# Optimization experiments

Hardware: AMD Instinct MI355X
Metric: run time of the kernel (lower is better)

The kernel has to match this reference:

```python
import jax, jax.numpy as jnp
import numpy as np

HUGE_FLOAT = 1000.0
B, LATENT, N, EMB, NBOND = 256, 256, 64, 64, 5


def setup_inputs() -> dict:
    key = jax.random.key(0)
    ks = jax.random.split(key, 8)
    s1 = 1.0 / np.sqrt(LATENT)
    s2 = 1.0 / np.sqrt(2 * EMB)
    s3 = 1.0 / np.sqrt(EMB)
    return {
        "z": jax.random.normal(ks[0], (B, LATENT), dtype=jnp.float32),
        "num_real_atoms": jax.random.randint(ks[1], (B,), 1, N + 1, dtype=jnp.int32),
        "W_nodes": jax.random.uniform(ks[2], (LATENT, N * EMB), jnp.float32, -s1, s1),
        "b_nodes": jax.random.uniform(ks[3], (N * EMB,), jnp.float32, -s1, s1),
        "W1": jax.random.uniform(ks[4], (2 * EMB, EMB), jnp.float32, -s2, s2),
        "b1": jax.random.uniform(ks[5], (EMB,), jnp.float32, -s2, s2),
        "W2": jax.random.uniform(ks[6], (EMB, NBOND), jnp.float32, -s3, s3),
        "b2": jax.random.uniform(ks[7], (NBOND,), jnp.float32, -s3, s3),
    }


def reference(z, num_real_atoms, W_nodes, b_nodes, W1, b1, W2, b2):
    # z: (B, latent) -> node embeddings h: (B, N, emb)
    h = (z @ W_nodes + b_nodes).reshape(B, N, EMB)
    # edge MLP first layer on concat([h_i, h_j]) == h_i @ W1a + h_j @ W1b
    W1a, W1b = W1[:EMB], W1[EMB:]
    a = jnp.einsum("bne,ef->bnf", h, W1a)  # (B, N, emb)
    c = jnp.einsum("bne,ef->bnf", h, W1b)  # (B, N, emb)
    hidden = jax.nn.relu(a[:, :, None, :] + c[:, None, :, :] + b1)  # (B,N,N,emb)
    logits = jnp.einsum("bijf,fk->bijk", hidden, W2) + b2  # (B,N,N,5)
    # diagonal mask + padding mask (symmetric), constant fill per bond channel
    diag = jnp.eye(N, dtype=bool)  # (N,N)
    real = jnp.arange(N)[None, :] < num_real_atoms[:, None]  # (B,N)
    pad = ~real
    padding = pad[:, :, None] | pad[:, None, :]  # (B,N,N)
    mask = diag[None] | padding  # (B,N,N)
    fill = jnp.where(jnp.arange(NBOND) == NBOND - 1, HUGE_FLOAT, -HUGE_FLOAT).astype(logits.dtype)
    logits = jnp.where(mask[..., None], fill, logits)
    # symmetrize over node pair dims
    return 0.5 * (logits + jnp.swapaxes(logits, 1, 2))
```

## Files before the change

### kernel.cpp

```cpp
#include <hip/hip_runtime.h>
#include <hip/hip_bf16.h>

#define HUGEF 1000.0f

typedef __hip_bfloat16 bf16;

__device__ __forceinline__ float b2f(bf16 x) { return __bfloat162float(x); }

__global__ __launch_bounds__(256) void k_hac(
    const float* __restrict__ z, const float* __restrict__ Wn,
    const float* __restrict__ bn, const float* __restrict__ W1,
    const float* __restrict__ b1, bf16* __restrict__ a_ws,
    bf16* __restrict__ c_ws)
{
    __shared__ float buf0[64][68];
    __shared__ float buf1[64][68];
    __shared__ float buf2[64][68];

    const int t = threadIdx.x;
    const int tx = t & 15, ty = t >> 4;
    const int atom = blockIdx.x;
    const int m0 = blockIdx.y * 64;
    const int n0 = atom * 64;

    float acc[4][4] = {};
    for (int k0 = 0; k0 < 256; k0 += 64) {
        __syncthreads();
        #pragma unroll
        for (int r = 0; r < 4; ++r) {
            int q = t + 256 * r;
            int m = q >> 4, kk = (q & 15) * 4;
            *(float4*)&buf0[m][kk] = *(const float4*)&z[(m0 + m) * 256 + k0 + kk];
        }
        #pragma unroll
        for (int r = 0; r < 4; ++r) {
            int q = t + 256 * r;
            int k = q >> 4, nn = (q & 15) * 4;
            *(float4*)&buf1[k][nn] = *(const float4*)&Wn[(k0 + k) * 4096 + n0 + nn];
        }
        __syncthreads();
        for (int k = 0; k < 64; ++k) {
            float4 bv = *(const float4*)&buf1[k][tx * 4];
            float bb[4] = {bv.x, bv.y, bv.z, bv.w};
            float aa[4];
            #pragma unroll
            for (int i = 0; i < 4; ++i) aa[i] = buf0[ty * 4 + i][k];
            #pragma unroll
            for (int i = 0; i < 4; ++i)
                #pragma unroll
                for (int jj = 0; jj < 4; ++jj) acc[i][jj] += aa[i] * bb[jj];
        }
    }
    __syncthreads();

    {
        float bnv[4];
        #pragma unroll
        for (int jj = 0; jj < 4; ++jj) bnv[jj] = bn[n0 + tx * 4 + jj];
        #pragma unroll
        for (int i = 0; i < 4; ++i)
            #pragma unroll
            for (int jj = 0; jj < 4; ++jj)
                buf2[ty * 4 + i][tx * 4 + jj] = acc[i][jj] + bnv[jj];
        #pragma unroll
        for (int r = 0; r < 4; ++r) {
            int q = t + 256 * r;
            int e = q >> 4, ff = (q & 15) * 4;
            *(float4*)&buf0[e][ff] = *(const float4*)&W1[4 * q];
            *(float4*)&buf1[e][ff] = *(const float4*)&W1[4096 + 4 * q];
        }
    }
    __syncthreads();

    float aacc[4][4] = {}, cacc[4][4] = {};
    const int b0 = ty * 4, f0 = tx * 4;
    for (int e = 0; e < 64; ++e) {
        float4 wa = *(const float4*)&buf0[e][f0];
        float4 wb = *(const float4*)&buf1[e][f0];
        float wav[4] = {wa.x, wa.y, wa.z, wa.w};
        float wbv[4] = {wb.x, wb.y, wb.z, wb.w};
        #pragma unroll
        for (int i = 0; i < 4; ++i) {
            float hv = buf2[b0 + i][e];
            #pragma unroll
            for (int jj = 0; jj < 4; ++jj) {
                aacc[i][jj] += hv * wav[jj];
                cacc[i][jj] += hv * wbv[jj];
            }
        }
    }
    float b1v[4];
    #pragma unroll
    for (int jj = 0; jj < 4; ++jj) b1v[jj] = b1[f0 + jj];
    #pragma unroll
    for (int i = 0; i < 4; ++i) {
        int bi = m0 + b0 + i;
        int idx = bi * 4096 + n0 + f0;
        ushort4 av, cv;
        av.x = __bfloat16_as_ushort(__float2bfloat16(aacc[i][0] + b1v[0]));
        av.y = __bfloat16_as_ushort(__float2bfloat16(aacc[i][1] + b1v[1]));
        av.z = __bfloat16_as_ushort(__float2bfloat16(aacc[i][2] + b1v[2]));
        av.w = __bfloat16_as_ushort(__float2bfloat16(aacc[i][3] + b1v[3]));
        cv.x = __bfloat16_as_ushort(__float2bfloat16(cacc[i][0]));
        cv.y = __bfloat16_as_ushort(__float2bfloat16(cacc[i][1]));
        cv.z = __bfloat16_as_ushort(__float2bfloat16(cacc[i][2]));
        cv.w = __bfloat16_as_ushort(__float2bfloat16(cacc[i][3]));
        *(ushort4*)&a_ws[idx] = av;
        *(ushort4*)&c_ws[idx] = cv;
    }
}

__global__ __launch_bounds__(256) void k_pairs(
    const bf16* __restrict__ a_ws, const bf16* __restrict__ c_ws,
    const int* __restrict__ nra, const float* __restrict__ W2,
    const float* __restrict__ b2, float* __restrict__ out)
{
    __shared__ float as[64][68];
    __shared__ float cs[64][68];
    __shared__ float w2t[5][68];

    const int t = threadIdx.x;
    const int bid = blockIdx.x;
    const int b = bid >> 2;
    const int ic = bid & 3;
    const int n = nra[b];

    #pragma unroll
    for (int r = 0; r < 4; ++r) {
        int q = t + 256 * r;
        int atom = q >> 4, ff = (q & 15) * 4;
        ushort4 av = *(const ushort4*)&a_ws[b * 4096 + 4 * q];
        ushort4 cv = *(const ushort4*)&c_ws[b * 4096 + 4 * q];
        as[atom][ff + 0] = b2f(__ushort_as_bfloat16(av.x));
        as[atom][ff + 1] = b2f(__ushort_as_bfloat16(av.y));
        as[atom][ff + 2] = b2f(__ushort_as_bfloat16(av.z));
        as[atom][ff + 3] = b2f(__ushort_as_bfloat16(av.w));
        cs[atom][ff + 0] = b2f(__ushort_as_bfloat16(cv.x));
        cs[atom][ff + 1] = b2f(__ushort_as_bfloat16(cv.y));
        cs[atom][ff + 2] = b2f(__ushort_as_bfloat16(cv.z));
        cs[atom][ff + 3] = b2f(__ushort_as_bfloat16(cv.w));
    }
    if (t < 64) {
        #pragma unroll
        for (int k = 0; k < 5; ++k) w2t[k][t] = W2[t * 5 + k];
    }
    float b2v[5];
    #pragma unroll
    for (int k = 0; k < 5; ++k) b2v[k] = b2[k];
    __syncthreads();

    const int j = t & 63;
    const int wq = t >> 6;
    const float fillv[5] = {-HUGEF, -HUGEF, -HUGEF, -HUGEF, HUGEF};

    #pragma unroll 1
    for (int q = 0; q < 4; ++q) {
        const int i = ic * 16 + wq * 4 + q;
        float* op = out + ((b * 64 + i) * 64 + j) * 5;
        if (i >= n) {
            #pragma unroll
            for (int k = 0; k < 5; ++k) op[k] = fillv[k];
            continue;
        }
        float acc[5] = {0.f, 0.f, 0.f, 0.f, 0.f};
        for (int f4 = 0; f4 < 64; f4 += 4) {
            float4 ai = *(const float4*)&as[i][f4];
            float4 ci = *(const float4*)&cs[i][f4];
            float4 aj = *(const float4*)&as[j][f4];
            float4 cj = *(const float4*)&cs[j][f4];
            float s0 = fmaxf(ai.x + cj.x, 0.f) + fmaxf(aj.x + ci.x, 0.f);
            float s1 = fmaxf(ai.y + cj.y, 0.f) + fmaxf(aj.y + ci.y, 0.f);
            float s2 = fmaxf(ai.z + cj.z, 0.f) + fmaxf(aj.z + ci.z, 0.f);
            float s3 = fmaxf(ai.w + cj.w, 0.f) + fmaxf(aj.w + ci.w, 0.f);
            #pragma unroll
            for (int k = 0; k < 5; ++k) {
                float4 w = *(const float4*)&w2t[k][f4];
                acc[k] += s0 * w.x + s1 * w.y + s2 * w.z + s3 * w.w;
            }
        }
        const bool masked = (j == i) || (j >= n);
        #pragma unroll
        for (int k = 0; k < 5; ++k) {
            float v = masked ? fillv[k] : (0.5f * acc[k] + b2v[k]);
            op[k] = v;
        }
    }
}

extern "C" void kernel_launch(void* const* d_in, const int* in_sizes, int n_in,
                              void* d_out, int out_size, void* d_ws, size_t ws_size,
                              hipStream_t stream)
{
    const float* z  = (const float*)d_in[0];
    const int*   nra = (const int*)d_in[1];
    const float* Wn = (const float*)d_in[2];
    const float* bn = (const float*)d_in[3];
    const float* W1 = (const float*)d_in[4];
    const float* b1 = (const float*)d_in[5];
    const float* W2 = (const float*)d_in[6];
    const float* b2 = (const float*)d_in[7];
    float* out = (float*)d_out;

    bf16* a_ws = (bf16*)d_ws;
    bf16* c_ws = a_ws + 256 * 4096;

    hipLaunchKernelGGL(k_hac, dim3(64, 4), dim3(256), 0, stream,
                       z, Wn, bn, W1, b1, a_ws, c_ws);
    hipLaunchKernelGGL(k_pairs, dim3(1024), dim3(256), 0, stream,
                       a_ws, c_ws, nra, W2, b2, out);
}
```

Measured before the change: 118.4 us.

## Prefetch GEMM tiles into registers, transpose smem for float4 reads, block pair loop

In the node/edge GEMM kernel, the next z and W_nodes tiles are prefetched into registers while the current tile is computed. z and h are stored transposed in shared memory so the inner loops can use float4 loads instead of strided scalar loads, and the inner loops are unrolled. In the pair kernel, each thread now handles four i-rows together, so the j-row and W2 loads are shared across them. Fully padded row groups exit early, and launch bounds request 4 blocks per CU. The cost is more registers per thread and bank conflicts from the transposed scalar shared-memory stores.

```diff
diff --git a/kernel.cpp b/kernel.cpp
--- a/kernel.cpp
+++ b/kernel.cpp
@@ -13,9 +13,9 @@
     const float* __restrict__ b1, bf16* __restrict__ a_ws,
     bf16* __restrict__ c_ws)
 {
-    __shared__ float buf0[64][68];
-    __shared__ float buf1[64][68];
-    __shared__ float buf2[64][68];
+    __shared__ __align__(16) float buf0[64][68];
+    __shared__ __align__(16) float buf1[64][68];
+    __shared__ __align__(16) float buf2[64][68];
 
     const int t = threadIdx.x;
     const int tx = t & 15, ty = t >> 4;
@@ -23,6 +23,16 @@
     const int m0 = blockIdx.y * 64;
     const int n0 = atom * 64;
 
+    float4 zr[4], wr[4];
+    #pragma unroll
+    for (int r = 0; r < 4; ++r) {
+        int q = t + 256 * r;
+        int m = q >> 4, kk = (q & 15) * 4;
+        zr[r] = *(const float4*)&z[(m0 + m) * 256 + 0 + kk];
+        int k = q >> 4, nn = (q & 15) * 4;
+        wr[r] = *(const float4*)&Wn[(0 + k) * 4096 + n0 + nn];
+    }
+
     float acc[4][4] = {};
     for (int k0 = 0; k0 < 256; k0 += 64) {
         __syncthreads();
@@ -30,21 +40,30 @@
         for (int r = 0; r < 4; ++r) {
             int q = t + 256 * r;
             int m = q >> 4, kk = (q & 15) * 4;
-            *(float4*)&buf0[m][kk] = *(const float4*)&z[(m0 + m) * 256 + k0 + kk];
-        }
-        #pragma unroll
-        for (int r = 0; r < 4; ++r) {
-            int q = t + 256 * r;
+            buf0[kk + 0][m] = zr[r].x;
+            buf0[kk + 1][m] = zr[r].y;
+            buf0[kk + 2][m] = zr[r].z;
+            buf0[kk + 3][m] = zr[r].w;
             int k = q >> 4, nn = (q & 15) * 4;
-            *(float4*)&buf1[k][nn] = *(const float4*)&Wn[(k0 + k) * 4096 + n0 + nn];
+            *(float4*)&buf1[k][nn] = wr[r];
+        }
+        if (k0 + 64 < 256) {
+            #pragma unroll
+            for (int r = 0; r < 4; ++r) {
+                int q = t + 256 * r;
+                int m = q >> 4, kk = (q & 15) * 4;
+                zr[r] = *(const float4*)&z[(m0 + m) * 256 + (k0 + 64) + kk];
+                int k = q >> 4, nn = (q & 15) * 4;
+                wr[r] = *(const float4*)&Wn[(k0 + 64 + k) * 4096 + n0 + nn];
+            }
         }
         __syncthreads();
+        #pragma unroll 4
         for (int k = 0; k < 64; ++k) {
+            float4 av = *(const float4*)&buf0[k][ty * 4];
             float4 bv = *(const float4*)&buf1[k][tx * 4];
+            float aa[4] = {av.x, av.y, av.z, av.w};
             float bb[4] = {bv.x, bv.y, bv.z, bv.w};
-            float aa[4];
-            #pragma unroll
-            for (int i = 0; i < 4; ++i) aa[i] = buf0[ty * 4 + i][k];
             #pragma unroll
             for (int i = 0; i < 4; ++i)
                 #pragma unroll
@@ -61,7 +80,7 @@
         for (int i = 0; i < 4; ++i)
             #pragma unroll
             for (int jj = 0; jj < 4; ++jj)
-                buf2[ty * 4 + i][tx * 4 + jj] = acc[i][jj] + bnv[jj];
+                buf2[tx * 4 + jj][ty * 4 + i] = acc[i][jj] + bnv[jj];
         #pragma unroll
         for (int r = 0; r < 4; ++r) {
             int q = t + 256 * r;
@@ -74,18 +93,20 @@
 
     float aacc[4][4] = {}, cacc[4][4] = {};
     const int b0 = ty * 4, f0 = tx * 4;
+    #pragma unroll 4
     for (int e = 0; e < 64; ++e) {
         float4 wa = *(const float4*)&buf0[e][f0];
         float4 wb = *(const float4*)&buf1[e][f0];
+        float4 hv4 = *(const float4*)&buf2[e][b0];
         float wav[4] = {wa.x, wa.y, wa.z, wa.w};
         float wbv[4] = {wb.x, wb.y, wb.z, wb.w};
+        float hv[4] = {hv4.x, hv4.y, hv4.z, hv4.w};
         #pragma unroll
         for (int i = 0; i < 4; ++i) {
-            float hv = buf2[b0 + i][e];
             #pragma unroll
             for (int jj = 0; jj < 4; ++jj) {
-                aacc[i][jj] += hv * wav[jj];
-                cacc[i][jj] += hv * wbv[jj];
+                aacc[i][jj] += hv[i] * wav[jj];
+                cacc[i][jj] += hv[i] * wbv[jj];
             }
         }
     }
@@ -110,14 +131,14 @@
     }
 }
 
-__global__ __launch_bounds__(256) void k_pairs(
+__global__ __launch_bounds__(256, 4) void k_pairs(
     const bf16* __restrict__ a_ws, const bf16* __restrict__ c_ws,
     const int* __restrict__ nra, const float* __restrict__ W2,
     const float* __restrict__ b2, float* __restrict__ out)
 {
-    __shared__ float as[64][68];
-    __shared__ float cs[64][68];
-    __shared__ float w2t[5][68];
+    __shared__ __align__(16) float as[64][68];
+    __shared__ __align__(16) float cs[64][68];
+    __shared__ __align__(16) float w2t[5][68];
 
     const int t = threadIdx.x;
     const int bid = blockIdx.x;
@@ -151,38 +172,56 @@
 
     const int j = t & 63;
     const int wq = t >> 6;
+    const int i0 = ic * 16 + wq * 4;
     const float fillv[5] = {-HUGEF, -HUGEF, -HUGEF, -HUGEF, HUGEF};
 
-    #pragma unroll 1
-    for (int q = 0; q < 4; ++q) {
-        const int i = ic * 16 + wq * 4 + q;
-        float* op = out + ((b * 64 + i) * 64 + j) * 5;
-        if (i >= n) {
+    if (i0 >= n) {
+        #pragma unroll
+        for (int r = 0; r < 4; ++r) {
+            float* op = out + ((b * 64 + i0 + r) * 64 + j) * 5;
             #pragma unroll
             for (int k = 0; k < 5; ++k) op[k] = fillv[k];
-            continue;
-        }
-        float acc[5] = {0.f, 0.f, 0.f, 0.f, 0.f};
-        for (int f4 = 0; f4 < 64; f4 += 4) {
-            float4 ai = *(const float4*)&as[i][f4];
-            float4 ci = *(const float4*)&cs[i][f4];
-            float4 aj = *(const float4*)&as[j][f4];
-            float4 cj = *(const float4*)&cs[j][f4];
+        }
+        return;
+    }
+
+    float acc[4][5] = {};
+    for (int f4 = 0; f4 < 64; f4 += 4) {
+        float4 aj = *(const float4*)&as[j][f4];
+        float4 cj = *(const float4*)&cs[j][f4];
+        float4 w0 = *(const float4*)&w2t[0][f4];
+        float4 w1 = *(const float4*)&w2t[1][f4];
+        float4 w2 = *(const float4*)&w2t[2][f4];
+        float4 w3 = *(const float4*)&w2t[3][f4];
+        float4 w4 = *(const float4*)&w2t[4][f4];
+        #pragma unroll
+        for (int r = 0; r < 4; ++r) {
+            float4 ai = *(const float4*)&as[i0 + r][f4];
+            float4 ci = *(const float4*)&cs[i0 + r][f4];
             float s0 = fmaxf(ai.x + cj.x, 0.f) + fmaxf(aj.x + ci.x, 0.f);
             float s1 = fmaxf(ai.y + cj.y, 0.f) + fmaxf(aj.y + ci.y, 0.f);
             float s2 = fmaxf(ai.z + cj.z, 0.f) + fmaxf(aj.z + ci.z, 0.f);
             float s3 = fmaxf(ai.w + cj.w, 0.f) + fmaxf(aj.w + ci.w, 0.f);
-            #pragma unroll
-            for (int k = 0; k < 5; ++k) {
-                float4 w = *(const float4*)&w2t[k][f4];
-                acc[k] += s0 * w.x + s1 * w.y + s2 * w.z + s3 * w.w;
-            }
-        }
-        const bool masked = (j == i) || (j >= n);
-        #pragma unroll
-        for (int k = 0; k < 5; ++k) {
-            float v = masked ? fillv[k] : (0.5f * acc[k] + b2v[k]);
-            op[k] = v;
+            acc[r][0] += s0 * w0.x + s1 * w0.y + s2 * w0.z + s3 * w0.w;
+            acc[r][1] += s0 * w1.x + s1 * w1.y + s2 * w1.z + s3 * w1.w;
+            acc[r][2] += s0 * w2.x + s1 * w2.y + s2 * w2.z + s3 * w2.w;
+            acc[r][3] += s0 * w3.x + s1 * w3.y + s2 * w3.z + s3 * w3.w;
+            acc[r][4] += s0 * w4.x + s1 * w4.y + s2 * w4.z + s3 * w4.w;
+        }
+    }
+
+    #pragma unroll
+    for (int r = 0; r < 4; ++r) {
+        const int i = i0 + r;
+        float* op = out + ((b * 64 + i) * 64 + j) * 5;
+        if (i >= n) {
+            #pragma unroll
+            for (int k = 0; k < 5; ++k) op[k] = fillv[k];
+        } else {
+            const bool masked = (j == i) || (j >= n);
+            #pragma unroll
+            for (int k = 0; k < 5; ++k)
+                op[k] = masked ? fillv[k] : (0.5f * acc[r][k] + b2v[k]);
         }
     }
 }
```

Result: faster. 115.8 us (-2.2%).
